# Performance work log

Hardware: AMD Instinct MI355X
Metric: run time of the kernel (lower is better)

Reference implementation:

```python
import jax, jax.numpy as jnp
import numpy as np

B, S, D = 4, 2048, 1024
NH, HD = 16, 64  # num_heads, head_dim; NH*HD == D


def setup_inputs() -> dict:
    key = jax.random.key(0)
    ks = jax.random.split(key, 10)
    s = 0.02
    return {
        "x": jax.random.normal(ks[0], (B, S, D), dtype=jnp.float32),
        "attention_mask": jnp.zeros((B, 1, 1, S), dtype=jnp.float32),
        "Wq": jax.random.normal(ks[1], (D, D), dtype=jnp.float32) * s,
        "bq": jnp.zeros((D,), dtype=jnp.float32),
        "Wk": jax.random.normal(ks[2], (D, D), dtype=jnp.float32) * s,
        "bk": jnp.zeros((D,), dtype=jnp.float32),
        "Wv": jax.random.normal(ks[3], (D, D), dtype=jnp.float32) * s,
        "bv": jnp.zeros((D,), dtype=jnp.float32),
        "Wo": jax.random.normal(ks[4], (D, D), dtype=jnp.float32) * s,
        "bo": jnp.zeros((D,), dtype=jnp.float32),
    }


def _heads(t):
    # [B,S,D] -> [B,NH,S,HD]
    return t.reshape(B, S, NH, HD).transpose(0, 2, 1, 3)


def reference(x, attention_mask, Wq, bq, Wk, bk, Wv, bv, Wo, bo):
    q = _heads(x @ Wq + bq)
    k = _heads(x @ Wk + bk)
    v = _heads(x @ Wv + bv)
    scores = jnp.einsum("bhqd,bhkd->bhqk", q, k) / jnp.sqrt(jnp.float32(HD))
    scores = scores + attention_mask
    attn = jax.nn.softmax(scores, axis=-1)  # dropout p=0 -> identity
    ctx = jnp.einsum("bhqk,bhkd->bhqd", attn, v)
    ctx = ctx.transpose(0, 2, 1, 3).reshape(B, S, D)
    return ctx @ Wo + bo
```

## Files before the change

### kernel.cpp

```cpp
#include <hip/hip_runtime.h>
#include <cstdint>
#include <cstddef>

typedef unsigned short u16;
typedef __attribute__((ext_vector_type(8))) __bf16 bf16x8;
typedef __attribute__((ext_vector_type(4))) float f32x4;
typedef __attribute__((ext_vector_type(16))) float f32x16;
typedef __attribute__((ext_vector_type(2))) uint32_t u32x2;
typedef __attribute__((ext_vector_type(4))) float float4v;

#define BATCH 4
#define S_LEN 2048
#define DMODEL 1024
#define NHEAD 16
#define HDIM 64
#define MROWS (BATCH * S_LEN)
#define LOG2E 1.4426950408889634f
#define SC_L (0.125f * LOG2E)

__device__ __forceinline__ u16 f2bf(float f) {
  uint32_t u = __float_as_uint(f);
  u += 0x7fffu + ((u >> 16) & 1u);
  return (u16)(u >> 16);
}

#if __has_builtin(__builtin_amdgcn_cvt_pk_bf16_f32)
__device__ __forceinline__ uint32_t packbf2(float a, float b) {
  auto t = __builtin_amdgcn_cvt_pk_bf16_f32(a, b);
  uint32_t u;
  __builtin_memcpy(&u, &t, 4);
  return u;
}
#else
__device__ __forceinline__ uint32_t packbf2(float a, float b) {
  uint32_t ua = __float_as_uint(a) + 0x8000u;
  uint32_t ub = __float_as_uint(b) + 0x8000u;
  return (ub & 0xFFFF0000u) | (ua >> 16);
}
#endif

#if __has_builtin(__builtin_amdgcn_exp2f)
#define EXP2(x) __builtin_amdgcn_exp2f(x)
#else
#define EXP2(x) exp2f(x)
#endif

typedef __attribute__((address_space(1))) void gvoid_t;
typedef __attribute__((address_space(3))) void svoid_t;
__device__ __forceinline__ void gl_lds16(const void* g, void* s) {
  __builtin_amdgcn_global_load_lds((gvoid_t*)g, (svoid_t*)s, 16, 0, 0);
}

#define NB_CVT (MROWS * DMODEL / 4 / 256)
__global__ __launch_bounds__(256) void prep_kernel(const float4v* __restrict__ x,
                                                   u32x2* __restrict__ xb,
                                                   const float* __restrict__ W0,
                                                   const float* __restrict__ W1,
                                                   const float* __restrict__ W2,
                                                   const float* __restrict__ W3,
                                                   u16* __restrict__ Wall) {
  __shared__ float tile[32][33];
  const int bid = blockIdx.x;
  const int tid = threadIdx.x;
  if (bid < NB_CVT) {
    const int i = bid * 256 + tid;
    float4v v = x[i];
    u32x2 o;
    o.x = packbf2(v.x, v.y);
    o.y = packbf2(v.z, v.w);
    xb[i] = o;
    return;
  }
  const int r = bid - NB_CVT;
  const int z = r >> 10;
  const int rem = r & 1023;
  const float* W = (z == 0) ? W0 : (z == 1) ? W1 : (z == 2) ? W2 : W3;
  u16* Wt = Wall + (size_t)z * DMODEL * DMODEL;
  const int n0 = (rem & 31) * 32, k0 = (rem >> 5) * 32;
  const int xx = tid & 31, y = tid >> 5;
  for (int yy = y; yy < 32; yy += 8)
    tile[yy][xx] = W[(size_t)(k0 + yy) * DMODEL + n0 + xx];
  __syncthreads();
  for (int yy = y; yy < 32; yy += 8)
    Wt[(size_t)(n0 + yy) * DMODEL + k0 + xx] = f2bf(tile[xx][yy]);
}

template <int MODE>
__global__ __launch_bounds__(256) void gemm128(const u16* __restrict__ A,
                                               const u16* __restrict__ Bt,
                                               const float* __restrict__ b0,
                                               const float* __restrict__ b1,
                                               const float* __restrict__ b2,
                                               void* __restrict__ o0,
                                               void* __restrict__ o1,
                                               void* __restrict__ o2) {
  __shared__ u16 As[2 * 128 * 32];
  __shared__ u16 Bs[2 * 128 * 32];
  const int tid = threadIdx.x;
  const int wid = tid >> 6;
  const int lane = tid & 63;
  const int l16 = lane & 15;
  const int g4 = lane >> 4;
  const int m0 = blockIdx.x * 128;
  const int n0 = blockIdx.y * 128;
  const int wm = (wid & 1) * 64;
  const int wn = (wid >> 1) * 64;

  const int srow = tid >> 2;
  const int sk = (tid & 3) * 8;
  const u16* gA = A + (size_t)(m0 + srow) * DMODEL + sk;
  const u16* gB = Bt + (size_t)(n0 + srow) * DMODEL + sk;
  char* sA = (char*)As + wid * 1024;
  char* sB = (char*)Bs + wid * 1024;

  f32x4 acc[4][4];
#pragma unroll
  for (int i = 0; i < 4; ++i)
#pragma unroll
    for (int j = 0; j < 4; ++j) acc[i][j] = (f32x4){0.f, 0.f, 0.f, 0.f};

  for (int k0 = 0; k0 < DMODEL; k0 += 64) {
    __syncthreads();
    gl_lds16(gA + k0, sA);
    gl_lds16(gA + (size_t)64 * DMODEL + k0, sA + 4096);
    gl_lds16(gB + k0, sB);
    gl_lds16(gB + (size_t)64 * DMODEL + k0, sB + 4096);
    gl_lds16(gA + k0 + 32, sA + 8192);
    gl_lds16(gA + (size_t)64 * DMODEL + k0 + 32, sA + 12288);
    gl_lds16(gB + k0 + 32, sB + 8192);
    gl_lds16(gB + (size_t)64 * DMODEL + k0 + 32, sB + 12288);
    __syncthreads();

#pragma unroll
    for (int kk = 0; kk < 2; ++kk) {
      const u16* Ab = As + kk * 4096;
      const u16* Bb = Bs + kk * 4096;
      bf16x8 af[4], bfr[4];
#pragma unroll
      for (int i = 0; i < 4; ++i)
        af[i] = *(const bf16x8*)(Ab + (wm + i * 16 + l16) * 32 + g4 * 8);
#pragma unroll
      for (int j = 0; j < 4; ++j)
        bfr[j] = *(const bf16x8*)(Bb + (wn + j * 16 + l16) * 32 + g4 * 8);
#pragma unroll
      for (int i = 0; i < 4; ++i)
#pragma unroll
        for (int j = 0; j < 4; ++j)
          acc[i][j] = __builtin_amdgcn_mfma_f32_16x16x32_bf16(af[i], bfr[j],
                                                              acc[i][j], 0, 0, 0);
    }
  }

  const int seg = n0 >> 10;
  const float* bp = (MODE == 1 || seg == 0) ? b0 : (seg == 1 ? b1 : b2);
  void* op = (MODE == 1 || seg == 0) ? o0 : (seg == 1 ? o1 : o2);

#pragma unroll
  for (int i = 0; i < 4; ++i) {
#pragma unroll
    for (int j = 0; j < 4; ++j) {
      const int coll = n0 + wn + j * 16 + l16;
      const int cseg = coll & 1023;
      const float bval = bp[cseg];
#pragma unroll
      for (int r = 0; r < 4; ++r) {
        const int rowg = m0 + wm + i * 16 + g4 * 4 + r;
        const float v = acc[i][j][r] + bval;
        if (MODE == 0) {
          const int b = rowg >> 11, s = rowg & (S_LEN - 1);
          const int h = cseg >> 6, d = cseg & (HDIM - 1);
          if (seg == 2) {
            ((u16*)op)[(((size_t)(b * NHEAD + h) * HDIM + d) << 11) + s] = f2bf(v);
          } else {
            ((u16*)op)[((size_t)((b * NHEAD + h) * S_LEN + s) << 6) + d] = f2bf(v);
          }
        } else {
          ((float*)op)[(size_t)rowg * DMODEL + cseg] = v;
        }
      }
    }
  }
}

__global__ __launch_bounds__(256, 2) void attn4_kernel(const u16* __restrict__ Q,
                                                       const u16* __restrict__ K,
                                                       const u16* __restrict__ Vt,
                                                       const float* __restrict__ mask,
                                                       u16* __restrict__ ctx) {
  __shared__ u16 Ks[64 * 72];
  __shared__ u16 Vs[64 * 72];

  const int tid = threadIdx.x;
  const int wid = tid >> 6;
  const int lane = tid & 63;
  const int l32 = lane & 31;
  const int hi = lane >> 5;
  const int flat = blockIdx.y * gridDim.x + blockIdx.x;
  const int nf = (flat & 7) * 64 + (flat >> 3);
  const int bx = nf & 7;
  const int bh = nf >> 3;
  const int b = bh >> 4;
  const int h = bh & 15;
  const int qw0 = bx * 256 + wid * 64;

  const u16* Qbase = Q + (size_t)bh * S_LEN * HDIM;
  bf16x8 aq[2][4];
#pragma unroll
  for (int qh = 0; qh < 2; ++qh)
#pragma unroll
    for (int c = 0; c < 4; ++c)
      aq[qh][c] = *(const bf16x8*)(Qbase + (size_t)(qw0 + qh * 32 + l32) * HDIM +
                                   c * 16 + hi * 8);

  union { u16 s[8]; bf16x8 v; } onesu;
#pragma unroll
  for (int i = 0; i < 8; ++i) onesu.s[i] = 0x3F80;
  const bf16x8 onesv = onesu.v;

  const f32x16 z16 = {};
  f32x16 oacc[2][2] = {};
  f32x16 lacc[2] = {};

  const int srow = tid >> 3;
  const int scol = (tid & 7) * 8;
  const int keyg = scol >> 4;
  const int todd = (scol >> 3) & 1;
  const int vkb = keyg * 16 + todd * 4;
  const u16* Kg = K + (size_t)bh * S_LEN * HDIM + (size_t)srow * HDIM + scol;
  const u16* Vg = Vt + (size_t)bh * HDIM * S_LEN + (size_t)srow * S_LEN + scol;
  const float* mrow = mask + (size_t)b * S_LEN;

  for (int kt = 0; kt < S_LEN; kt += 64) {
    bf16x8 kv0 = *(const bf16x8*)(Kg + (size_t)kt * HDIM);
    bf16x8 kv1 = *(const bf16x8*)(Kg + (size_t)(kt + 32) * HDIM);
    union { bf16x8 v; uint32_t u[4]; } vv0, vv1;
    vv0.v = *(const bf16x8*)(Vg + kt);
    vv1.v = *(const bf16x8*)(Vg + (size_t)32 * S_LEN + kt);
    __syncthreads();
    *(bf16x8*)(Ks + srow * 72 + scol) = kv0;
    *(bf16x8*)(Ks + (srow + 32) * 72 + scol) = kv1;
    *(u32x2*)(Vs + srow * 72 + vkb) = (u32x2){vv0.u[0], vv0.u[1]};
    *(u32x2*)(Vs + srow * 72 + vkb + 8) = (u32x2){vv0.u[2], vv0.u[3]};
    *(u32x2*)(Vs + (srow + 32) * 72 + vkb) = (u32x2){vv1.u[0], vv1.u[1]};
    *(u32x2*)(Vs + (srow + 32) * 72 + vkb + 8) = (u32x2){vv1.u[2], vv1.u[3]};
    __syncthreads();

    uint32_t P[2][2][8];
#pragma unroll
    for (int T = 0; T < 2; ++T) {
      bf16x8 kf[4];
#pragma unroll
      for (int c = 0; c < 4; ++c)
        kf[c] = *(const bf16x8*)(Ks + (T * 32 + l32) * 72 + c * 16 + hi * 8);
      f32x4 m4[4];
#pragma unroll
      for (int tq = 0; tq < 4; ++tq) {
        f32x4 mr = *(const f32x4*)(mrow + kt + T * 32 + tq * 8 + hi * 4);
        m4[tq] = mr * LOG2E;
      }
#pragma unroll
      for (int qh = 0; qh < 2; ++qh) {
        f32x16 s = __builtin_amdgcn_mfma_f32_32x32x16_bf16(kf[0], aq[qh][0], z16, 0, 0, 0);
#pragma unroll
        for (int c = 1; c < 4; ++c)
          s = __builtin_amdgcn_mfma_f32_32x32x16_bf16(kf[c], aq[qh][c], s, 0, 0, 0);
#pragma unroll
        for (int tq = 0; tq < 4; ++tq) {
          float p0 = EXP2(fmaf(s[tq * 4 + 0], SC_L, m4[tq][0]));
          float p1 = EXP2(fmaf(s[tq * 4 + 1], SC_L, m4[tq][1]));
          float p2 = EXP2(fmaf(s[tq * 4 + 2], SC_L, m4[tq][2]));
          float p3 = EXP2(fmaf(s[tq * 4 + 3], SC_L, m4[tq][3]));
          P[T][qh][tq * 2] = packbf2(p0, p1);
          P[T][qh][tq * 2 + 1] = packbf2(p2, p3);
        }
      }
    }

#pragma unroll
    for (int c = 0; c < 4; ++c) {
      const int T = c >> 1, half = c & 1;
      bf16x8 vf[2];
#pragma unroll
      for (int dh = 0; dh < 2; ++dh)
        vf[dh] = *(const bf16x8*)(Vs + (dh * 32 + l32) * 72 + c * 16 + hi * 8);
#pragma unroll
      for (int qh = 0; qh < 2; ++qh) {
        union { uint32_t u[4]; bf16x8 v; } pf;
#pragma unroll
        for (int e = 0; e < 4; ++e) pf.u[e] = P[T][qh][half * 4 + e];
        oacc[qh][0] = __builtin_amdgcn_mfma_f32_32x32x16_bf16(pf.v, vf[0], oacc[qh][0], 0, 0, 0);
        oacc[qh][1] = __builtin_amdgcn_mfma_f32_32x32x16_bf16(pf.v, vf[1], oacc[qh][1], 0, 0, 0);
        lacc[qh] = __builtin_amdgcn_mfma_f32_32x32x16_bf16(pf.v, onesv, lacc[qh], 0, 0, 0);
      }
    }
  }

#pragma unroll
  for (int qh = 0; qh < 2; ++qh) {
#pragma unroll
    for (int reg = 0; reg < 16; ++reg) {
      const int q = qw0 + qh * 32 + (reg & 3) + 8 * (reg >> 2) + 4 * hi;
      const float inv = 1.0f / lacc[qh][reg];
      u16* cp = ctx + ((size_t)(b * S_LEN + q) * NHEAD + h) * HDIM;
      cp[l32] = f2bf(oacc[qh][0][reg] * inv);
      cp[32 + l32] = f2bf(oacc[qh][1][reg] * inv);
    }
  }
}

extern "C" void kernel_launch(void* const* d_in, const int* in_sizes, int n_in,
                              void* d_out, int out_size, void* d_ws, size_t ws_size,
                              hipStream_t stream) {
  const float* x = (const float*)d_in[0];
  const float* mask = (const float*)d_in[1];
  const float* Wq = (const float*)d_in[2];
  const float* bq = (const float*)d_in[3];
  const float* Wk = (const float*)d_in[4];
  const float* bk = (const float*)d_in[5];
  const float* Wv = (const float*)d_in[6];
  const float* bv = (const float*)d_in[7];
  const float* Wo = (const float*)d_in[8];
  const float* bo = (const float*)d_in[9];
  float* out = (float*)d_out;

  char* ws = (char*)d_ws;
  size_t off = 0;
  u16* xb = (u16*)(ws + off);    off += (size_t)MROWS * DMODEL * 2;
  u16* wall = (u16*)(ws + off);  off += (size_t)4 * DMODEL * DMODEL * 2;
  u16* Qh = (u16*)(ws + off);    off += (size_t)MROWS * DMODEL * 2;
  u16* Kh = (u16*)(ws + off);    off += (size_t)MROWS * DMODEL * 2;
  u16* Vtb = (u16*)(ws + off);   off += (size_t)MROWS * DMODEL * 2;
  u16* ctxb = (u16*)(ws + off);  off += (size_t)MROWS * DMODEL * 2;
  (void)ws_size; (void)in_sizes; (void)n_in; (void)out_size;

  prep_kernel<<<dim3(NB_CVT + 4096), dim3(256), 0, stream>>>(
      (const float4v*)x, (u32x2*)xb, Wq, Wk, Wv, Wo, wall);

  gemm128<0><<<dim3(MROWS / 128, 3 * DMODEL / 128), dim3(256), 0, stream>>>(
      xb, wall, bq, bk, bv, (void*)Qh, (void*)Kh, (void*)Vtb);

  attn4_kernel<<<dim3(S_LEN / 256, BATCH * NHEAD), dim3(256), 0, stream>>>(Qh, Kh, Vtb, mask, ctxb);

  gemm128<1><<<dim3(MROWS / 128, DMODEL / 128), dim3(256), 0, stream>>>(
      ctxb, wall + (size_t)3 * DMODEL * DMODEL, bo, bo, bo, (void*)out, (void*)out, (void*)out);
}
```

Baseline: 291.2 us.

## Triple-buffer GEMM K-loop with async LDS loads and pre-scale mask by log2e

The GEMM main loop goes from a load-then-compute pattern with two barriers per 64-wide K step to a three-stage ring of 32-wide K tiles. Loads run two tiles ahead, with vmcnt waits and one barrier per step, so global-to-LDS transfers overlap the MFMA work. Separately, the prep kernel now multiplies the attention mask by log2e once into a workspace buffer, which removes a per-tile multiply in the attention inner loop. The ring raises LDS use to 48KB per GEMM block, which may lower occupancy, and it relies on hand-placed waitcnt and barrier ordering being correct.

New measurement: 293.1 us. Within noise of the previous version (+0.6%).

```diff
diff --git a/kernel.cpp b/kernel.cpp
--- a/kernel.cpp
+++ b/kernel.cpp
@@ -52,13 +52,16 @@
 }
 
 #define NB_CVT (MROWS * DMODEL / 4 / 256)
+#define NB_W   4096
 __global__ __launch_bounds__(256) void prep_kernel(const float4v* __restrict__ x,
                                                    u32x2* __restrict__ xb,
                                                    const float* __restrict__ W0,
                                                    const float* __restrict__ W1,
                                                    const float* __restrict__ W2,
                                                    const float* __restrict__ W3,
-                                                   u16* __restrict__ Wall) {
+                                                   u16* __restrict__ Wall,
+                                                   const float* __restrict__ mask,
+                                                   float* __restrict__ mL) {
   __shared__ float tile[32][33];
   const int bid = blockIdx.x;
   const int tid = threadIdx.x;
@@ -69,6 +72,11 @@
     o.x = packbf2(v.x, v.y);
     o.y = packbf2(v.z, v.w);
     xb[i] = o;
+    return;
+  }
+  if (bid >= NB_CVT + NB_W) {
+    const int i = (bid - NB_CVT - NB_W) * 256 + tid;
+    mL[i] = mask[i] * LOG2E;
     return;
   }
   const int r = bid - NB_CVT;
@@ -94,8 +102,8 @@
                                                void* __restrict__ o0,
                                                void* __restrict__ o1,
                                                void* __restrict__ o2) {
-  __shared__ u16 As[2 * 128 * 32];
-  __shared__ u16 Bs[2 * 128 * 32];
+  __shared__ u16 As[3][128 * 32];
+  __shared__ u16 Bs[3][128 * 32];
   const int tid = threadIdx.x;
   const int wid = tid >> 6;
   const int lane = tid & 63;
@@ -110,8 +118,6 @@
   const int sk = (tid & 3) * 8;
   const u16* gA = A + (size_t)(m0 + srow) * DMODEL + sk;
   const u16* gB = Bt + (size_t)(n0 + srow) * DMODEL + sk;
-  char* sA = (char*)As + wid * 1024;
-  char* sB = (char*)Bs + wid * 1024;
 
   f32x4 acc[4][4];
 #pragma unroll
@@ -119,37 +125,60 @@
 #pragma unroll
     for (int j = 0; j < 4; ++j) acc[i][j] = (f32x4){0.f, 0.f, 0.f, 0.f};
 
-  for (int k0 = 0; k0 < DMODEL; k0 += 64) {
-    __syncthreads();
-    gl_lds16(gA + k0, sA);
-    gl_lds16(gA + (size_t)64 * DMODEL + k0, sA + 4096);
-    gl_lds16(gB + k0, sB);
-    gl_lds16(gB + (size_t)64 * DMODEL + k0, sB + 4096);
-    gl_lds16(gA + k0 + 32, sA + 8192);
-    gl_lds16(gA + (size_t)64 * DMODEL + k0 + 32, sA + 12288);
-    gl_lds16(gB + k0 + 32, sB + 8192);
-    gl_lds16(gB + (size_t)64 * DMODEL + k0 + 32, sB + 12288);
-    __syncthreads();
-
-#pragma unroll
-    for (int kk = 0; kk < 2; ++kk) {
-      const u16* Ab = As + kk * 4096;
-      const u16* Bb = Bs + kk * 4096;
-      bf16x8 af[4], bfr[4];
-#pragma unroll
-      for (int i = 0; i < 4; ++i)
-        af[i] = *(const bf16x8*)(Ab + (wm + i * 16 + l16) * 32 + g4 * 8);
+#define STAGE_T(c, t)                                                   \
+  {                                                                     \
+    char* sa = (char*)As + (c) * 8192 + wid * 1024;                     \
+    char* sb = (char*)Bs + (c) * 8192 + wid * 1024;                     \
+    gl_lds16(gA + (t) * 32, sa);                                        \
+    gl_lds16(gA + (size_t)64 * DMODEL + (t) * 32, sa + 4096);           \
+    gl_lds16(gB + (t) * 32, sb);                                        \
+    gl_lds16(gB + (size_t)64 * DMODEL + (t) * 32, sb + 4096);           \
+  }
+
+  const int NT = DMODEL / 32;
+
+  STAGE_T(0, 0)
+  STAGE_T(1, 1)
+  asm volatile("s_waitcnt vmcnt(4)" ::: "memory");
+  __builtin_amdgcn_sched_barrier(0);
+  __builtin_amdgcn_s_barrier();
+  __builtin_amdgcn_sched_barrier(0);
+
+#pragma unroll
+  for (int r = 0; r < 32; ++r) {
+    const int c = r % 3;
+    if (r + 2 < NT) {
+      const int c2 = (r + 2) % 3;
+      STAGE_T(c2, r + 2)
+    }
+
+    const u16* Ab = &As[c][0];
+    const u16* Bb = &Bs[c][0];
+    bf16x8 af[4], bfr[4];
+#pragma unroll
+    for (int i = 0; i < 4; ++i)
+      af[i] = *(const bf16x8*)(Ab + (wm + i * 16 + l16) * 32 + g4 * 8);
+#pragma unroll
+    for (int j = 0; j < 4; ++j)
+      bfr[j] = *(const bf16x8*)(Bb + (wn + j * 16 + l16) * 32 + g4 * 8);
+#pragma unroll
+    for (int i = 0; i < 4; ++i)
 #pragma unroll
       for (int j = 0; j < 4; ++j)
-        bfr[j] = *(const bf16x8*)(Bb + (wn + j * 16 + l16) * 32 + g4 * 8);
-#pragma unroll
-      for (int i = 0; i < 4; ++i)
-#pragma unroll
-        for (int j = 0; j < 4; ++j)
-          acc[i][j] = __builtin_amdgcn_mfma_f32_16x16x32_bf16(af[i], bfr[j],
-                                                              acc[i][j], 0, 0, 0);
-    }
-  }
+        acc[i][j] = __builtin_amdgcn_mfma_f32_16x16x32_bf16(af[i], bfr[j],
+                                                            acc[i][j], 0, 0, 0);
+
+    if (r + 1 < NT) {
+      if (r + 2 < NT)
+        asm volatile("s_waitcnt vmcnt(4)" ::: "memory");
+      else
+        asm volatile("s_waitcnt vmcnt(0)" ::: "memory");
+      __builtin_amdgcn_sched_barrier(0);
+      __builtin_amdgcn_s_barrier();
+      __builtin_amdgcn_sched_barrier(0);
+    }
+  }
+#undef STAGE_T
 
   const int seg = n0 >> 10;
   const float* bp = (MODE == 1 || seg == 0) ? b0 : (seg == 1 ? b1 : b2);
@@ -185,7 +214,7 @@
 __global__ __launch_bounds__(256, 2) void attn4_kernel(const u16* __restrict__ Q,
                                                        const u16* __restrict__ K,
                                                        const u16* __restrict__ Vt,
-                                                       const float* __restrict__ mask,
+                                                       const float* __restrict__ maskL,
                                                        u16* __restrict__ ctx) {
   __shared__ u16 Ks[64 * 72];
   __shared__ u16 Vs[64 * 72];
@@ -228,7 +257,7 @@
   const int vkb = keyg * 16 + todd * 4;
   const u16* Kg = K + (size_t)bh * S_LEN * HDIM + (size_t)srow * HDIM + scol;
   const u16* Vg = Vt + (size_t)bh * HDIM * S_LEN + (size_t)srow * S_LEN + scol;
-  const float* mrow = mask + (size_t)b * S_LEN;
+  const float* mrow = maskL + (size_t)b * S_LEN;
 
   for (int kt = 0; kt < S_LEN; kt += 64) {
     bf16x8 kv0 = *(const bf16x8*)(Kg + (size_t)kt * HDIM);
@@ -254,10 +283,8 @@
         kf[c] = *(const bf16x8*)(Ks + (T * 32 + l32) * 72 + c * 16 + hi * 8);
       f32x4 m4[4];
 #pragma unroll
-      for (int tq = 0; tq < 4; ++tq) {
-        f32x4 mr = *(const f32x4*)(mrow + kt + T * 32 + tq * 8 + hi * 4);
-        m4[tq] = mr * LOG2E;
-      }
+      for (int tq = 0; tq < 4; ++tq)
+        m4[tq] = *(const f32x4*)(mrow + kt + T * 32 + tq * 8 + hi * 4);
 #pragma unroll
       for (int qh = 0; qh < 2; ++qh) {
         f32x16 s = __builtin_amdgcn_mfma_f32_32x32x16_bf16(kf[0], aq[qh][0], z16, 0, 0, 0);
@@ -331,15 +358,16 @@
   u16* Kh = (u16*)(ws + off);    off += (size_t)MROWS * DMODEL * 2;
   u16* Vtb = (u16*)(ws + off);   off += (size_t)MROWS * DMODEL * 2;
   u16* ctxb = (u16*)(ws + off);  off += (size_t)MROWS * DMODEL * 2;
+  float* mL = (float*)(ws + off); off += (size_t)BATCH * S_LEN * 4;
   (void)ws_size; (void)in_sizes; (void)n_in; (void)out_size;
 
-  prep_kernel<<<dim3(NB_CVT + 4096), dim3(256), 0, stream>>>(
-      (const float4v*)x, (u32x2*)xb, Wq, Wk, Wv, Wo, wall);
+  prep_kernel<<<dim3(NB_CVT + NB_W + BATCH * S_LEN / 256), dim3(256), 0, stream>>>(
+      (const float4v*)x, (u32x2*)xb, Wq, Wk, Wv, Wo, wall, mask, mL);
 
   gemm128<0><<<dim3(MROWS / 128, 3 * DMODEL / 128), dim3(256), 0, stream>>>(
       xb, wall, bq, bk, bv, (void*)Qh, (void*)Kh, (void*)Vtb);
 
-  attn4_kernel<<<dim3(S_LEN / 256, BATCH * NHEAD), dim3(256), 0, stream>>>(Qh, Kh, Vtb, mask, ctxb);
+  attn4_kernel<<<dim3(S_LEN / 256, BATCH * NHEAD), dim3(256), 0, stream>>>(Qh, Kh, Vtb, mL, ctxb);
 
   gemm128<1><<<dim3(MROWS / 128, DMODEL / 128), dim3(256), 0, stream>>>(
       ctxb, wall + (size_t)3 * DMODEL * DMODEL, bo, bo, bo, (void*)out, (void*)out, (void*)out);
```
